# Performance work log

Measured on AMD Instinct MI355X. Metric: run time of the kernel, lower is better.

The kernel has to match this reference:

```python
import jax, jax.numpy as jnp
import numpy as np

RADIUS = 0.05
HMIN = -0.02
HMAX = 0.04
NSAMPLE = 64
NPOINT = 1024


def fps(xyz, npoint):
    # Farthest point sampling, deterministic start at index 0.
    # xyz: (B, N, 3) -> (B, npoint) int32
    B, N, _ = xyz.shape

    def step(carry, _):
        dist, farthest = carry
        centroid = jnp.take_along_axis(xyz, farthest[:, None, None], axis=1)  # (B,1,3)
        d = jnp.sum((xyz - centroid) ** 2, axis=-1)  # (B,N)
        dist = jnp.minimum(dist, d)
        nxt = jnp.argmax(dist, axis=-1).astype(jnp.int32)
        return (dist, nxt), farthest

    init = (jnp.full((B, N), 1e10, xyz.dtype), jnp.zeros((B,), jnp.int32))
    _, idxs = jax.lax.scan(step, init, None, length=npoint)
    return idxs.T  # (B, npoint)


def cylinder_query(xyz, new_xyz, rot9, hmin, hmax, nsample):
    # Faithful to the original torch code, INCLUDING its r2-shadowing bug:
    # the radial threshold is rot[..., 2], not radius**2.
    B, N, _ = xyz.shape
    _, P, _ = new_xyz.shape
    R = rot9.reshape(B, P, 3, 3)
    diff = xyz[:, None, :, :] - new_xyz[:, :, None, :]          # (B,P,N,3)
    rot_d = jnp.einsum('bpnk,bpkc->bpnc', diff, R)               # (B,P,N,3)
    d2 = rot_d[..., 1] ** 2 + rot_d[..., 2] ** 2                 # (B,P,N)
    thresh = rot9[..., 2][:, :, None]                            # bug replicated
    mask = (d2 < thresh) & (rot_d[..., 0] > hmin) & (rot_d[..., 0] < hmax)

    k = jnp.arange(N, dtype=jnp.int32)

    def first_nsample(m):  # m: (N,) bool -> (nsample,) int32, zero-padded
        pos = jnp.where(m, jnp.cumsum(m) - 1, nsample)
        return jnp.zeros((nsample,), jnp.int32).at[pos].set(k, mode='drop')

    return jax.vmap(jax.vmap(first_nsample))(mask)  # (B,P,nsample)


def group(feats, idx):
    # feats: (B, C, N), idx: (B, P, S) -> (B, C, P, S)
    return jax.vmap(lambda f, i: f[:, i])(feats, idx)


def setup_inputs() -> dict:
    key = jax.random.key(0)
    ks = jax.random.split(key, 6)
    B, N, C = 4, 4096, 256
    xyz = jax.random.uniform(ks[0], (B, N, 3), dtype=jnp.float32)
    features = jax.random.normal(ks[1], (B, C, N), dtype=jnp.float32)
    rot = jax.random.uniform(ks[2], (B, NPOINT, 9), dtype=jnp.float32)
    W1 = jax.random.normal(ks[3], (256, 3 + C), dtype=jnp.float32) * 0.05
    b1 = jnp.zeros((256,), jnp.float32)
    W2 = jax.random.normal(ks[4], (256, 256), dtype=jnp.float32) * 0.05
    b2 = jnp.zeros((256,), jnp.float32)
    return {"xyz": xyz, "features": features, "rot": rot,
            "W1": W1, "b1": b1, "W2": W2, "b2": b2}


def reference(xyz, features, rot, W1, b1, W2, b2):
    B = xyz.shape[0]
    # 1) FPS seeds
    fps_idx = fps(xyz, NPOINT)                                        # (B,P)
    new_xyz = jnp.take_along_axis(xyz, fps_idx[:, :, None], axis=1)   # (B,P,3)
    # 2) cylinder neighbor query
    idx = cylinder_query(xyz, new_xyz, rot, HMIN, HMAX, NSAMPLE)      # (B,P,S)
    # 3) grouping (xyz recentred + rotated into cylinder frame)
    xyz_t = jnp.transpose(xyz, (0, 2, 1))                             # (B,3,N)
    grouped_xyz = group(xyz_t, idx)                                   # (B,3,P,S)
    grouped_xyz = grouped_xyz - jnp.transpose(new_xyz, (0, 2, 1))[:, :, :, None]
    R = rot.reshape(B, NPOINT, 3, 3)
    g = jnp.transpose(grouped_xyz, (0, 2, 3, 1))                      # (B,P,S,3)
    g = jnp.einsum('bpsk,bpkc->bpsc', g, R)
    grouped_xyz = jnp.transpose(g, (0, 3, 1, 2))                      # (B,3,P,S)
    grouped_feat = group(features, idx)                               # (B,C,P,S)
    x = jnp.concatenate([grouped_xyz, grouped_feat], axis=1)          # (B,3+C,P,S)
    # 4) shared pointwise MLP + max-pool over samples
    h = jax.nn.relu(jnp.einsum('oc,bcps->bops', W1, x) + b1[None, :, None, None])
    h = jax.nn.relu(jnp.einsum('oc,bcps->bops', W2, h) + b2[None, :, None, None])
    return jnp.max(h, axis=-1)                                        # (B,256,P)
```

## Files before the change

### kernel.cpp

```cpp
#include <hip/hip_runtime.h>
#include <hip/hip_bf16.h>

#define B_ 4
#define N_ 4096
#define C_ 256
#define P_ 1024
#define S_ 64
#define HST 264

typedef __attribute__((ext_vector_type(8))) short short8;
typedef __attribute__((ext_vector_type(4))) float f32x4;

__device__ __forceinline__ float rn_mul(float a, float b){ return __fmul_rn(a,b); }
__device__ __forceinline__ float rn_add(float a, float b){ return __fadd_rn(a,b); }
__device__ __forceinline__ float rn_sub(float a, float b){ return __fsub_rn(a,b); }

__device__ __forceinline__ unsigned short f2bf(float x){
  union { float f; unsigned u; } v; v.f = x;
  unsigned r = v.u + 0x7fffu + ((v.u >> 16) & 1u);
  return (unsigned short)(r >> 16);
}

#define DPPMAX(m, ctrl) \
  m = fmaxf(m, __int_as_float(__builtin_amdgcn_update_dpp(0, __float_as_int(m), ctrl, 0xF, 0xF, true)))

__global__ __launch_bounds__(256, 1) void pre_kernel(
    const float* __restrict__ xyz, float* __restrict__ newXyz,
    const float* __restrict__ f, unsigned short* __restrict__ ft,
    const float* __restrict__ W1, const float* __restrict__ W2,
    unsigned short* __restrict__ Wp1, unsigned short* __restrict__ Wp2)
{
  __shared__ __align__(16) char shm[N_*3*4 + 8*16];
  const int gid = blockIdx.x;
  const int t = threadIdx.x;

  if (gid < B_){
    float* xl = (float*)shm;
    float4* cand = (float4*)(shm + N_*3*4);
    const int b = gid;
    const int lane = t & 63, w = t >> 6;
    const float* xb = xyz + (size_t)b*N_*3;
    {
      float4* dst = (float4*)xl; const float4* src = (const float4*)xb;
      for (int i = t; i < N_*3/4; i += 256) dst[i] = src[i];
    }
    __syncthreads();
    float px[16], py[16], pz[16], dist[16];
    {
      float buf[48];
      #pragma unroll
      for (int i=0;i<12;i++){
        const float4 v = *(const float4*)&xl[t*48 + i*4];
        buf[i*4+0]=v.x; buf[i*4+1]=v.y; buf[i*4+2]=v.z; buf[i*4+3]=v.w;
      }
      #pragma unroll
      for (int j=0;j<16;j++){
        px[j]=buf[j*3+0]; py[j]=buf[j*3+1]; pz[j]=buf[j*3+2];
        dist[j] = 1e10f;
      }
    }
    float cx = xl[0], cy = xl[1], cz = xl[2];
    for (int it=0; it<P_; ++it){
      if (t == 0){
        float* nz = newXyz + ((size_t)b*P_ + it)*3;
        nz[0]=cx; nz[1]=cy; nz[2]=cz;
      }
      float bestv = -1.f; int bestj = 0;
      #pragma unroll
      for (int j=0;j<16;j++){
        const float dx = rn_sub(px[j],cx), dy = rn_sub(py[j],cy), dz = rn_sub(pz[j],cz);
        const float d  = rn_add(rn_add(rn_mul(dx,dx), rn_mul(dy,dy)), rn_mul(dz,dz));
        const float nd = fminf(dist[j], d);
        dist[j] = nd;
        if (nd > bestv){ bestv = nd; bestj = j; }
      }
      float m = bestv;
      DPPMAX(m, 0x111);
      DPPMAX(m, 0x112);
      DPPMAX(m, 0x114);
      DPPMAX(m, 0x118);
      DPPMAX(m, 0x142);
      DPPMAX(m, 0x143);
      const float ms = __int_as_float(__builtin_amdgcn_readlane(__float_as_int(m), 63));
      const unsigned long long bal = __ballot(bestv == ms);
      const int winlane = __ffsll((long long)bal) - 1;
      const int widx = __builtin_amdgcn_readlane(t*16 + bestj, winlane) & ~15;
      const int wj   = __builtin_amdgcn_readlane(bestj, winlane);
      const int pb = it & 1;
      if (lane == 0){
        const float* cp = xl + (size_t)(widx + wj)*3;
        cand[pb*4 + w] = make_float4(ms, cp[0], cp[1], cp[2]);
      }
      __syncthreads();
      const float4 c0 = cand[pb*4+0], c1 = cand[pb*4+1], c2 = cand[pb*4+2], c3 = cand[pb*4+3];
      float fv = c0.x; cx = c0.y; cy = c0.z; cz = c0.w;
      if (c1.x > fv){ fv = c1.x; cx = c1.y; cy = c1.z; cz = c1.w; }
      if (c2.x > fv){ fv = c2.x; cx = c2.y; cy = c2.z; cz = c2.w; }
      if (c3.x > fv){ fv = c3.x; cx = c3.y; cy = c3.z; cz = c3.w; }
    }
  } else if (gid < B_ + 256){
    const int o = gid - B_;
    Wp1[o*288 + t] = f2bf(W1[o*259 + 3 + t]);
    if (t < 32){
      float v = (t < 3) ? W1[o*259 + t] : 0.f;
      Wp1[o*288 + 256 + t] = f2bf(v);
    }
    Wp2[o*256 + t] = f2bf(W2[o*256 + t]);
  } else {
    const int idx = gid - (B_ + 256);
    const int nx = idx & 127;
    const int cyi = (idx >> 7) & 7;
    const int bz = idx >> 10;
    float (*tile)[33] = (float (*)[33])shm;
    const int n0 = nx*32, c0 = cyi*32;
    const int tx = t & 31, ty = t >> 5;
    #pragma unroll
    for (int j=0;j<4;j++)
      tile[ty + j*8][tx] = f[((size_t)bz*C_ + (size_t)(c0+ty+j*8))*N_ + n0 + tx];
    __syncthreads();
    #pragma unroll
    for (int j=0;j<4;j++)
      ft[((size_t)bz*N_ + (size_t)(n0+ty+j*8))*C_ + c0 + tx] = f2bf(tile[tx][ty + j*8]);
  }
}

__global__ __launch_bounds__(256) void query_kernel(const float* __restrict__ xyz,
                                                    const float* __restrict__ rot,
                                                    const float* __restrict__ newXyz,
                                                    int* __restrict__ sIdx,
                                                    unsigned short* __restrict__ sRotPk)
{
  const int lane = threadIdx.x & 63;
  const int bp = blockIdx.x * 4 + (threadIdx.x >> 6);
  const int b = bp >> 10;
  const float* xb = xyz + (size_t)b*N_*3;
  const float* r9 = rot + (size_t)bp*9;
  const float R0=r9[0],R1=r9[1],R2=r9[2],R3=r9[3],R4=r9[4],R5=r9[5],R6=r9[6],R7=r9[7],R8=r9[8];
  const float nx=newXyz[bp*3+0], ny=newXyz[bp*3+1], nz=newXyz[bp*3+2];
  const float thr = R2;
  int* oI = sIdx + (size_t)bp*S_;
  unsigned short* oR = sRotPk + (size_t)bp*S_*8;
  int filled = 0;
  float p0r0=0.f, p0r1=0.f, p0r2=0.f;
  for (int base = 0; base < N_; base += 64){
    const int n = base + lane;
    const float dx = rn_sub(xb[n*3+0], nx);
    const float dy = rn_sub(xb[n*3+1], ny);
    const float dz = rn_sub(xb[n*3+2], nz);
    const float r0 = rn_add(rn_add(rn_mul(dx,R0), rn_mul(dy,R3)), rn_mul(dz,R6));
    const float r1 = rn_add(rn_add(rn_mul(dx,R1), rn_mul(dy,R4)), rn_mul(dz,R7));
    const float r2 = rn_add(rn_add(rn_mul(dx,R2), rn_mul(dy,R5)), rn_mul(dz,R8));
    if (base == 0){
      p0r0 = __shfl(r0, 0, 64); p0r1 = __shfl(r1, 0, 64); p0r2 = __shfl(r2, 0, 64);
    }
    const float d2 = rn_add(rn_mul(r1,r1), rn_mul(r2,r2));
    const bool m = (d2 < thr) & (r0 > -0.02f) & (r0 < 0.04f);
    const unsigned long long bal = __ballot(m);
    const int before = (int)__popcll(bal & ((1ull << lane) - 1ull));
    const int slot = filled + before;
    if (m && slot < S_){
      oI[slot] = n;
      uint4 u;
      u.x = (unsigned)f2bf(r0) | ((unsigned)f2bf(r1) << 16);
      u.y = (unsigned)f2bf(r2);
      u.z = 0u; u.w = 0u;
      *(uint4*)(oR + slot*8) = u;
    }
    filled += (int)__popcll(bal);
    if (filled >= S_) break;
  }
  if (filled < S_){
    const int slot = filled + lane;
    if (slot < S_){
      oI[slot] = 0;
      uint4 u;
      u.x = (unsigned)f2bf(p0r0) | ((unsigned)f2bf(p0r1) << 16);
      u.y = (unsigned)f2bf(p0r2);
      u.z = 0u; u.w = 0u;
      *(uint4*)(oR + slot*8) = u;
    }
  }
}

__global__ __launch_bounds__(256,2) void mlp_kernel(
    const unsigned short* __restrict__ featT,
    const int* __restrict__ sIdx,
    const unsigned short* __restrict__ sRotPk,
    const unsigned short* __restrict__ Wp1,
    const float* __restrict__ b1,
    const unsigned short* __restrict__ Wp2,
    const float* __restrict__ b2,
    float* __restrict__ out)
{
  __shared__ unsigned short Hlds[2][64*HST];
  const int bid = blockIdx.x;
  const int pp = (bid & 7) * 256 + (bid >> 3);
  const int bp0 = pp*2, bp1 = bp0 + 1;
  const int b = bp0 >> 10, p0 = bp0 & 1023;
  const int t = threadIdx.x;
  const int w = t >> 6, l = t & 63;
  const int l15 = l & 15, q = l >> 4;

  unsigned rowOff[8];
  #pragma unroll
  for (int st=0; st<8; ++st){
    const int bpX = (st < 4) ? bp0 : bp1;
    const int s = (st & 3)*16 + l15;
    const int row = sIdx[(size_t)bpX*S_ + s];
    rowOff[st] = (unsigned)(((b*N_ + row)*C_ + q*8) * 2);
  }
  const char* fbase = (const char*)featT;

  f32x4 acc[4][8];
  #pragma unroll
  for (int at=0; at<4; ++at){
    const float4 bv = *(const float4*)(b1 + w*64 + at*16 + q*4);
    #pragma unroll
    for (int st=0; st<8; ++st){
      acc[at][st][0]=bv.x; acc[at][st][1]=bv.y; acc[at][st][2]=bv.z; acc[at][st][3]=bv.w;
    }
  }

  const unsigned short* wb1 = Wp1 + (size_t)(w*64 + l15)*288 + q*8;
  #pragma unroll
  for (int ks=0; ks<8; ++ks){
    short8 a[4], x[8];
    #pragma unroll
    for (int at=0; at<4; ++at) a[at] = *(const short8*)(wb1 + at*16*288 + ks*32);
    #pragma unroll
    for (int st=0; st<8; ++st) x[st] = *(const short8*)(fbase + rowOff[st] + ks*64);
    #pragma unroll
    for (int at=0; at<4; ++at)
      #pragma unroll
      for (int st=0; st<8; ++st)
        acc[at][st] = __builtin_amdgcn_mfma_f32_16x16x32_bf16(a[at], x[st], acc[at][st], 0,0,0);
  }
  {
    short8 a[4], x[8];
    #pragma unroll
    for (int at=0; at<4; ++at) a[at] = *(const short8*)(wb1 + at*16*288 + 8*32);
    #pragma unroll
    for (int st=0; st<8; ++st){
      short8 v = (short8){0,0,0,0,0,0,0,0};
      if (q == 0){
        const int bpX = (st < 4) ? bp0 : bp1;
        const int s = (st & 3)*16 + l15;
        v = *(const short8*)(sRotPk + ((size_t)bpX*S_ + s)*8);
      }
      x[st] = v;
    }
    #pragma unroll
    for (int at=0; at<4; ++at)
      #pragma unroll
      for (int st=0; st<8; ++st)
        acc[at][st] = __builtin_amdgcn_mfma_f32_16x16x32_bf16(a[at], x[st], acc[at][st], 0,0,0);
  }

  #pragma unroll
  for (int at=0; at<4; ++at)
    #pragma unroll
    for (int st=0; st<8; ++st){
      const int s = (st & 3)*16 + l15;
      const int o = w*64 + at*16 + q*4;
      const unsigned h0 = f2bf(fmaxf(acc[at][st][0], 0.f));
      const unsigned h1 = f2bf(fmaxf(acc[at][st][1], 0.f));
      const unsigned h2 = f2bf(fmaxf(acc[at][st][2], 0.f));
      const unsigned h3 = f2bf(fmaxf(acc[at][st][3], 0.f));
      uint2 u; u.x = h0 | (h1 << 16); u.y = h2 | (h3 << 16);
      *(uint2*)&Hlds[st >> 2][s*HST + o] = u;
    }
  __syncthreads();

  #pragma unroll
  for (int at=0; at<4; ++at){
    const float4 bv = *(const float4*)(b2 + w*64 + at*16 + q*4);
    #pragma unroll
    for (int st=0; st<8; ++st){
      acc[at][st][0]=bv.x; acc[at][st][1]=bv.y; acc[at][st][2]=bv.z; acc[at][st][3]=bv.w;
    }
  }
  const unsigned short* wb2 = Wp2 + (size_t)(w*64 + l15)*256 + q*8;
  #pragma unroll
  for (int ks=0; ks<8; ++ks){
    short8 a[4], h[8];
    #pragma unroll
    for (int at=0; at<4; ++at) a[at] = *(const short8*)(wb2 + at*16*256 + ks*32);
    #pragma unroll
    for (int st=0; st<8; ++st)
      h[st] = *(const short8*)&Hlds[st >> 2][((st & 3)*16 + l15)*HST + ks*32 + q*8];
    #pragma unroll
    for (int at=0; at<4; ++at)
      #pragma unroll
      for (int st=0; st<8; ++st)
        acc[at][st] = __builtin_amdgcn_mfma_f32_16x16x32_bf16(a[at], h[st], acc[at][st], 0,0,0);
  }

  #pragma unroll
  for (int g=0; g<2; ++g){
    const int p = p0 + g;
    #pragma unroll
    for (int at=0; at<4; ++at){
      #pragma unroll
      for (int r=0; r<4; ++r){
        float m = fmaxf(fmaxf(acc[at][g*4+0][r], acc[at][g*4+1][r]),
                        fmaxf(acc[at][g*4+2][r], acc[at][g*4+3][r]));
        m = fmaxf(m, __shfl_xor(m, 1, 64));
        m = fmaxf(m, __shfl_xor(m, 2, 64));
        m = fmaxf(m, __shfl_xor(m, 4, 64));
        m = fmaxf(m, __shfl_xor(m, 8, 64));
        m = fmaxf(m, 0.f);
        if (l15 == 0){
          const int o = w*64 + at*16 + q*4 + r;
          out[((size_t)b*256 + o)*P_ + p] = m;
        }
      }
    }
  }
}

extern "C" void kernel_launch(void* const* d_in, const int* in_sizes, int n_in,
                              void* d_out, int out_size, void* d_ws, size_t ws_size,
                              hipStream_t stream)
{
  const float* xyz  = (const float*)d_in[0];
  const float* feat = (const float*)d_in[1];
  const float* rot  = (const float*)d_in[2];
  const float* W1   = (const float*)d_in[3];
  const float* b1   = (const float*)d_in[4];
  const float* W2   = (const float*)d_in[5];
  const float* b2   = (const float*)d_in[6];
  float* out = (float*)d_out;

  char* ws = (char*)d_ws;
  unsigned short* featT = (unsigned short*)(ws);
  size_t off = (size_t)B_*N_*C_*2;
  float* newXyz = (float*)(ws + off); off += (size_t)B_*P_*3*4;
  int*   sIdx   = (int*)  (ws + off); off += (size_t)B_*P_*S_*4;
  unsigned short* sRotPk = (unsigned short*)(ws + off); off += (size_t)B_*P_*S_*8*2;
  unsigned short* Wp1 = (unsigned short*)(ws + off); off += (size_t)256*288*2;
  unsigned short* Wp2 = (unsigned short*)(ws + off); off += (size_t)256*256*2;
  (void)ws_size; (void)in_sizes; (void)n_in; (void)out_size;

  hipLaunchKernelGGL(pre_kernel,   dim3(B_ + 256 + 4096), dim3(256), 0, stream,
                     xyz, newXyz, feat, featT, W1, W2, Wp1, Wp2);
  hipLaunchKernelGGL(query_kernel, dim3(B_*P_/4),         dim3(256), 0, stream,
                     xyz, rot, newXyz, sIdx, sRotPk);
  hipLaunchKernelGGL(mlp_kernel,   dim3(B_*P_/2),         dim3(256), 0, stream,
                     featT, sIdx, sRotPk, Wp1, b1, Wp2, b2, out);
}
```

Baseline: 782.3 us.

## Fuse cylinder query into MLP kernel using shared-memory neighbor lists

Removes the separate query kernel and computes the neighbor indices and rotated offsets inside the MLP block. Two of the four waves scan the points for their centroid and write the results to LDS, followed by a block barrier. This saves one kernel launch and the global round trip for sIdx and sRotPk. In exchange, the MLP waves sit idle during the serial scan, and LDS use grows, which may reduce occupancy.

```diff
diff --git a/kernel.cpp b/kernel.cpp
--- a/kernel.cpp
+++ b/kernel.cpp
@@ -124,68 +124,11 @@
   }
 }
 
-__global__ __launch_bounds__(256) void query_kernel(const float* __restrict__ xyz,
-                                                    const float* __restrict__ rot,
-                                                    const float* __restrict__ newXyz,
-                                                    int* __restrict__ sIdx,
-                                                    unsigned short* __restrict__ sRotPk)
-{
-  const int lane = threadIdx.x & 63;
-  const int bp = blockIdx.x * 4 + (threadIdx.x >> 6);
-  const int b = bp >> 10;
-  const float* xb = xyz + (size_t)b*N_*3;
-  const float* r9 = rot + (size_t)bp*9;
-  const float R0=r9[0],R1=r9[1],R2=r9[2],R3=r9[3],R4=r9[4],R5=r9[5],R6=r9[6],R7=r9[7],R8=r9[8];
-  const float nx=newXyz[bp*3+0], ny=newXyz[bp*3+1], nz=newXyz[bp*3+2];
-  const float thr = R2;
-  int* oI = sIdx + (size_t)bp*S_;
-  unsigned short* oR = sRotPk + (size_t)bp*S_*8;
-  int filled = 0;
-  float p0r0=0.f, p0r1=0.f, p0r2=0.f;
-  for (int base = 0; base < N_; base += 64){
-    const int n = base + lane;
-    const float dx = rn_sub(xb[n*3+0], nx);
-    const float dy = rn_sub(xb[n*3+1], ny);
-    const float dz = rn_sub(xb[n*3+2], nz);
-    const float r0 = rn_add(rn_add(rn_mul(dx,R0), rn_mul(dy,R3)), rn_mul(dz,R6));
-    const float r1 = rn_add(rn_add(rn_mul(dx,R1), rn_mul(dy,R4)), rn_mul(dz,R7));
-    const float r2 = rn_add(rn_add(rn_mul(dx,R2), rn_mul(dy,R5)), rn_mul(dz,R8));
-    if (base == 0){
-      p0r0 = __shfl(r0, 0, 64); p0r1 = __shfl(r1, 0, 64); p0r2 = __shfl(r2, 0, 64);
-    }
-    const float d2 = rn_add(rn_mul(r1,r1), rn_mul(r2,r2));
-    const bool m = (d2 < thr) & (r0 > -0.02f) & (r0 < 0.04f);
-    const unsigned long long bal = __ballot(m);
-    const int before = (int)__popcll(bal & ((1ull << lane) - 1ull));
-    const int slot = filled + before;
-    if (m && slot < S_){
-      oI[slot] = n;
-      uint4 u;
-      u.x = (unsigned)f2bf(r0) | ((unsigned)f2bf(r1) << 16);
-      u.y = (unsigned)f2bf(r2);
-      u.z = 0u; u.w = 0u;
-      *(uint4*)(oR + slot*8) = u;
-    }
-    filled += (int)__popcll(bal);
-    if (filled >= S_) break;
-  }
-  if (filled < S_){
-    const int slot = filled + lane;
-    if (slot < S_){
-      oI[slot] = 0;
-      uint4 u;
-      u.x = (unsigned)f2bf(p0r0) | ((unsigned)f2bf(p0r1) << 16);
-      u.y = (unsigned)f2bf(p0r2);
-      u.z = 0u; u.w = 0u;
-      *(uint4*)(oR + slot*8) = u;
-    }
-  }
-}
-
 __global__ __launch_bounds__(256,2) void mlp_kernel(
+    const float* __restrict__ xyz,
+    const float* __restrict__ rot,
+    const float* __restrict__ newXyz,
     const unsigned short* __restrict__ featT,
-    const int* __restrict__ sIdx,
-    const unsigned short* __restrict__ sRotPk,
     const unsigned short* __restrict__ Wp1,
     const float* __restrict__ b1,
     const unsigned short* __restrict__ Wp2,
@@ -193,6 +136,8 @@
     float* __restrict__ out)
 {
   __shared__ unsigned short Hlds[2][64*HST];
+  __shared__ int sI[2][S_];
+  __shared__ unsigned short rotP[2][S_*8];
   const int bid = blockIdx.x;
   const int pp = (bid & 7) * 256 + (bid >> 3);
   const int bp0 = pp*2, bp1 = bp0 + 1;
@@ -201,12 +146,62 @@
   const int w = t >> 6, l = t & 63;
   const int l15 = l & 15, q = l >> 4;
 
+  if (w < 2){
+    const int g = w;
+    const int bp = bp0 + g;
+    const float* xb = xyz + (size_t)b*N_*3;
+    const float* r9 = rot + (size_t)bp*9;
+    const float R0=r9[0],R1=r9[1],R2=r9[2],R3=r9[3],R4=r9[4],R5=r9[5],R6=r9[6],R7=r9[7],R8=r9[8];
+    const float nx=newXyz[bp*3+0], ny=newXyz[bp*3+1], nz=newXyz[bp*3+2];
+    const float thr = R2;
+    int filled = 0;
+    float p0r0=0.f, p0r1=0.f, p0r2=0.f;
+    for (int base = 0; base < N_; base += 64){
+      const int n = base + l;
+      const float dx = rn_sub(xb[n*3+0], nx);
+      const float dy = rn_sub(xb[n*3+1], ny);
+      const float dz = rn_sub(xb[n*3+2], nz);
+      const float r0 = rn_add(rn_add(rn_mul(dx,R0), rn_mul(dy,R3)), rn_mul(dz,R6));
+      const float r1 = rn_add(rn_add(rn_mul(dx,R1), rn_mul(dy,R4)), rn_mul(dz,R7));
+      const float r2 = rn_add(rn_add(rn_mul(dx,R2), rn_mul(dy,R5)), rn_mul(dz,R8));
+      if (base == 0){
+        p0r0 = __shfl(r0, 0, 64); p0r1 = __shfl(r1, 0, 64); p0r2 = __shfl(r2, 0, 64);
+      }
+      const float d2 = rn_add(rn_mul(r1,r1), rn_mul(r2,r2));
+      const bool m = (d2 < thr) & (r0 > -0.02f) & (r0 < 0.04f);
+      const unsigned long long bal = __ballot(m);
+      const int before = (int)__popcll(bal & ((1ull << l) - 1ull));
+      const int slot = filled + before;
+      if (m && slot < S_){
+        sI[g][slot] = n;
+        uint4 u;
+        u.x = (unsigned)f2bf(r0) | ((unsigned)f2bf(r1) << 16);
+        u.y = (unsigned)f2bf(r2);
+        u.z = 0u; u.w = 0u;
+        *(uint4*)&rotP[g][slot*8] = u;
+      }
+      filled += (int)__popcll(bal);
+      if (filled >= S_) break;
+    }
+    if (filled < S_){
+      const int slot = filled + l;
+      if (slot < S_){
+        sI[g][slot] = 0;
+        uint4 u;
+        u.x = (unsigned)f2bf(p0r0) | ((unsigned)f2bf(p0r1) << 16);
+        u.y = (unsigned)f2bf(p0r2);
+        u.z = 0u; u.w = 0u;
+        *(uint4*)&rotP[g][slot*8] = u;
+      }
+    }
+  }
+  __syncthreads();
+
   unsigned rowOff[8];
   #pragma unroll
   for (int st=0; st<8; ++st){
-    const int bpX = (st < 4) ? bp0 : bp1;
     const int s = (st & 3)*16 + l15;
-    const int row = sIdx[(size_t)bpX*S_ + s];
+    const int row = sI[st >> 2][s];
     rowOff[st] = (unsigned)(((b*N_ + row)*C_ + q*8) * 2);
   }
   const char* fbase = (const char*)featT;
@@ -243,9 +238,8 @@
     for (int st=0; st<8; ++st){
       short8 v = (short8){0,0,0,0,0,0,0,0};
       if (q == 0){
-        const int bpX = (st < 4) ? bp0 : bp1;
         const int s = (st & 3)*16 + l15;
-        v = *(const short8*)(sRotPk + ((size_t)bpX*S_ + s)*8);
+        v = *(const short8*)&rotP[st >> 2][s*8];
       }
       x[st] = v;
     }
@@ -335,16 +329,12 @@
   unsigned short* featT = (unsigned short*)(ws);
   size_t off = (size_t)B_*N_*C_*2;
   float* newXyz = (float*)(ws + off); off += (size_t)B_*P_*3*4;
-  int*   sIdx   = (int*)  (ws + off); off += (size_t)B_*P_*S_*4;
-  unsigned short* sRotPk = (unsigned short*)(ws + off); off += (size_t)B_*P_*S_*8*2;
   unsigned short* Wp1 = (unsigned short*)(ws + off); off += (size_t)256*288*2;
   unsigned short* Wp2 = (unsigned short*)(ws + off); off += (size_t)256*256*2;
   (void)ws_size; (void)in_sizes; (void)n_in; (void)out_size;
 
-  hipLaunchKernelGGL(pre_kernel,   dim3(B_ + 256 + 4096), dim3(256), 0, stream,
+  hipLaunchKernelGGL(pre_kernel, dim3(B_ + 256 + 4096), dim3(256), 0, stream,
                      xyz, newXyz, feat, featT, W1, W2, Wp1, Wp2);
-  hipLaunchKernelGGL(query_kernel, dim3(B_*P_/4),         dim3(256), 0, stream,
-                     xyz, rot, newXyz, sIdx, sRotPk);
-  hipLaunchKernelGGL(mlp_kernel,   dim3(B_*P_/2),         dim3(256), 0, stream,
-                     featT, sIdx, sRotPk, Wp1, b1, Wp2, b2, out);
+  hipLaunchKernelGGL(mlp_kernel, dim3(B_*P_/2), dim3(256), 0, stream,
+                     xyz, rot, newXyz, featT, Wp1, b1, Wp2, b2, out);
 }
```

After: 814.6 us. 4.1% more time.
